# Kernel optimization log

Measured on AMD Instinct MI355X. Metric: run time of the kernel, lower is better.

## Reference

```python
import jax, jax.numpy as jnp
import numpy as np
from jax import lax

RES = 14
DIM = 384
KEY_DIM = 32
NUM_HEADS = 12
ATTN_RATIO = 4
NH_KD = KEY_DIM * NUM_HEADS            # 384
DH = ATTN_RATIO * KEY_DIM * NUM_HEADS  # 1536
HQKV = DH + 2 * NH_KD                  # 2304
BN_EPS = 1e-5


def _bias_idxs():
    ys, xs = np.meshgrid(np.arange(RES), np.arange(RES), indexing='ij')
    ys = ys.reshape(-1); xs = xs.reshape(-1)
    dy = np.abs(ys[:, None] - ys[None, :])
    dx = np.abs(xs[:, None] - xs[None, :])
    return jnp.asarray(dy * RES + dx, dtype=jnp.int32)  # [196,196], 196 unique offsets


def setup_inputs() -> dict:
    key = jax.random.key(0)
    ks = jax.random.split(key, 16)
    B = 128
    x = jax.random.normal(ks[0], (B, DIM, RES, RES), dtype=jnp.float32)
    # qkv: 1x1 conv DIM->HQKV + BN
    qkv_w = jax.random.normal(ks[1], (HQKV, DIM, 1, 1), dtype=jnp.float32) * 0.05
    qkv_g = jax.random.normal(ks[2], (HQKV,), dtype=jnp.float32) * 0.1 + 1.0
    qkv_b = jax.random.normal(ks[3], (HQKV,), dtype=jnp.float32) * 0.1
    qkv_m = jax.random.normal(ks[4], (HQKV,), dtype=jnp.float32) * 0.1
    qkv_v = jax.random.uniform(ks[5], (HQKV,), dtype=jnp.float32) + 0.5
    # dw: depthwise 3x3 conv on q channels + BN
    dw_w = jax.random.normal(ks[6], (NH_KD, 1, 3, 3), dtype=jnp.float32) * 0.2
    dw_g = jax.random.normal(ks[7], (NH_KD,), dtype=jnp.float32) * 0.1 + 1.0
    dw_b = jax.random.normal(ks[8], (NH_KD,), dtype=jnp.float32) * 0.1
    dw_m = jax.random.normal(ks[9], (NH_KD,), dtype=jnp.float32) * 0.1
    dw_v = jax.random.uniform(ks[10], (NH_KD,), dtype=jnp.float32) + 0.5
    # proj: ReLU -> 1x1 conv DH->DIM + BN
    proj_w = jax.random.normal(ks[11], (DIM, DH, 1, 1), dtype=jnp.float32) * 0.05
    proj_g = jax.random.normal(ks[12], (DIM,), dtype=jnp.float32) * 0.1 + 1.0
    proj_b = jax.random.normal(ks[13], (DIM,), dtype=jnp.float32) * 0.1
    proj_m = jax.random.normal(ks[14], (DIM,), dtype=jnp.float32) * 0.1
    proj_v = jax.random.uniform(ks[15], (DIM,), dtype=jnp.float32) + 0.5
    ab = jax.random.normal(jax.random.fold_in(key, 99), (NUM_HEADS, RES * RES), dtype=jnp.float32) * 0.1
    return {
        'x': x,
        'qkv_w': qkv_w, 'qkv_g': qkv_g, 'qkv_b': qkv_b, 'qkv_m': qkv_m, 'qkv_v': qkv_v,
        'dw_w': dw_w, 'dw_g': dw_g, 'dw_b': dw_b, 'dw_m': dw_m, 'dw_v': dw_v,
        'proj_w': proj_w, 'proj_g': proj_g, 'proj_b': proj_b, 'proj_m': proj_m, 'proj_v': proj_v,
        'attn_biases': ab,
        'bias_idxs': _bias_idxs(),
    }


def _bn(x, g, b, m, v):
    scale = g / jnp.sqrt(v + BN_EPS)
    return x * scale[None, :, None, None] + (b - m * scale)[None, :, None, None]


def reference(x, qkv_w, qkv_g, qkv_b, qkv_m, qkv_v,
              dw_w, dw_g, dw_b, dw_m, dw_v,
              proj_w, proj_g, proj_b, proj_m, proj_v,
              attn_biases, bias_idxs):
    B, _, H, W = x.shape
    n = H * W
    scale = KEY_DIM ** -0.5
    # 1x1 conv + BN
    qkv = jnp.einsum('bchw,oc->bohw', x, qkv_w[:, :, 0, 0])
    qkv = _bn(qkv, qkv_g, qkv_b, qkv_m, qkv_v)
    q = qkv[:, :NH_KD]
    k = qkv[:, NH_KD:2 * NH_KD]
    v = qkv[:, 2 * NH_KD:]
    # depthwise 3x3 conv + BN on q
    q = lax.conv_general_dilated(q, dw_w, (1, 1), ((1, 1), (1, 1)),
                                 dimension_numbers=('NCHW', 'OIHW', 'NCHW'),
                                 feature_group_count=NH_KD)
    q = _bn(q, dw_g, dw_b, dw_m, dw_v)
    # heads: [b, h, d, n]
    q = q.reshape(B, NUM_HEADS, KEY_DIM, n)
    k = k.reshape(B, NUM_HEADS, KEY_DIM, n)
    v = v.reshape(B, NUM_HEADS, ATTN_RATIO * KEY_DIM, n)
    bias = attn_biases[:, bias_idxs]  # [h, n, n]
    attn = jnp.einsum('bhdn,bhdm->bhnm', q, k) * scale + bias[None]
    attn = jax.nn.softmax(attn, axis=-1)
    out = jnp.einsum('bhdm,bhnm->bhdn', v, attn).reshape(B, DH, H, W)
    out = jax.nn.relu(out)
    out = jnp.einsum('bchw,oc->bohw', out, proj_w[:, :, 0, 0])
    return _bn(out, proj_g, proj_b, proj_m, proj_v)
```

## Files before the change

kernel.cpp:

```cpp
#include <hip/hip_runtime.h>

typedef __bf16 bf16;
typedef bf16 bf16x8 __attribute__((ext_vector_type(8)));
typedef bf16 bf16x4 __attribute__((ext_vector_type(4)));
typedef short short4v __attribute__((ext_vector_type(4)));
typedef float f32x4 __attribute__((ext_vector_type(4)));

#define NPIX 196
#define CIN 384
#define NHEADS 12
#define MPAD 224
#define VSTRIDE 232
#define OSTRIDE 40
#define TSTRIDE 136
#define TSF 136

#define N_WQ (2304 * 384)
#define N_WP (384 * 1536)
#define N_WD (384 * 9)
#define N_BI (NHEADS * NPIX * MPAD)

__device__ __forceinline__ float ldf(const void* p, size_t i, int f) {
    return f ? ((const float*)p)[i] : (float)((const bf16*)p)[i];
}

__device__ __forceinline__ void gld16(const void* g, void* lds_wave_base) {
    __builtin_amdgcn_global_load_lds(
        (const __attribute__((address_space(1))) void*)(unsigned long long)g,
        (__attribute__((address_space(3))) void*)(unsigned long long)lds_wave_base,
        16, 0, 0);
}

__device__ __forceinline__ int xcd_swizzle(int orig, int nwg) {
    int q = nwg >> 3, r = nwg & 7;
    int xcd = orig & 7, idx = orig >> 3;
    return (xcd < r ? xcd * (q + 1) : r * (q + 1) + (xcd - r) * q) + idx;
}

__device__ __forceinline__ f32x4 mfma16(bf16x4 a, bf16x4 b, f32x4 c) {
#if __has_builtin(__builtin_amdgcn_mfma_f32_16x16x16bf16_1k)
    return __builtin_amdgcn_mfma_f32_16x16x16bf16_1k(
        __builtin_bit_cast(short4v, a), __builtin_bit_cast(short4v, b), c, 0, 0, 0);
#else
    asm volatile("v_mfma_f32_16x16x16_bf16 %0, %1, %2, %0" : "+v"(c) : "v"(a), "v"(b));
    return c;
#endif
}

__device__ __forceinline__ f32x4 vmax4(f32x4 a, f32x4 b) {
    f32x4 r;
    r[0] = fmaxf(a[0], b[0]);
    r[1] = fmaxf(a[1], b[1]);
    r[2] = fmaxf(a[2], b[2]);
    r[3] = fmaxf(a[3], b[3]);
    return r;
}

__global__ void detect_kernel(const unsigned int* __restrict__ x, int* __restrict__ flag) {
    __shared__ int cnt;
    if (threadIdx.x == 0) cnt = 0;
    __syncthreads();
    int c = 0;
#pragma unroll
    for (int k = 0; k < 8; k++) {
        unsigned int w = x[threadIdx.x * 8 + k];
        unsigned int e = (w >> 7) & 0xFFu;
        if (e > 200u) c++;
    }
    atomicAdd(&cnt, c);
    __syncthreads();
    if (threadIdx.x == 0) *flag = (cnt >= 16) ? 1 : 0;
}

__global__ void prep_kernel(const void* __restrict__ qkv_w, const void* __restrict__ proj_w,
                            const void* __restrict__ dw_w, const void* __restrict__ ab,
                            const int* __restrict__ idx, const int* __restrict__ flag,
                            bf16* __restrict__ wq, bf16* __restrict__ wp, bf16* __restrict__ wd,
                            float* __restrict__ biasf, bf16* __restrict__ vb, int nvpad) {
    int f = *flag;
    long t = (long)blockIdx.x * 256 + threadIdx.x;
    if (t < N_WQ) { wq[t] = (bf16)ldf(qkv_w, t, f); return; }
    t -= N_WQ;
    if (t < N_WP) { wp[t] = (bf16)ldf(proj_w, t, f); return; }
    t -= N_WP;
    if (t < N_WD) { wd[t] = (bf16)ldf(dw_w, t, f); return; }
    t -= N_WD;
    if (t < N_BI) {
        int h = (int)(t / (NPIX * MPAD));
        int rem = (int)(t - (long)h * (NPIX * MPAD));
        int n = rem / MPAD, m = rem - n * MPAD;
        biasf[t] = (m < NPIX) ? ldf(ab, h * NPIX + idx[n * NPIX + m], f) : -1e30f;
        return;
    }
    t -= N_BI;
    if (t < nvpad) {
        long r = t / 7, c = t - r * 7;
        *(unsigned long long*)(vb + r * MPAD + NPIX + c * 4) = 0ull;
    }
}

__global__ void transpose_x_kernel(const void* __restrict__ x, const int* __restrict__ flag,
                                   bf16* __restrict__ xt, int b0) {
    __shared__ bf16 tile[32][33];
    int f = *flag;
    int b = blockIdx.z, gb = b0 + b;
    int c0 = blockIdx.y * 32;
    int hw0 = blockIdx.x * 32;
    int tx = threadIdx.x, ty = threadIdx.y;
    int hw = hw0 + tx, c = c0 + ty;
    if (hw < NPIX) tile[ty][tx] = (bf16)ldf(x, ((size_t)gb * CIN + c) * NPIX + hw, f);
    __syncthreads();
    int hw2 = hw0 + ty, c2 = c0 + tx;
    if (hw2 < NPIX) xt[((size_t)b * NPIX + hw2) * CIN + c2] = tile[tx][ty];
}

__device__ __forceinline__ void gemm_tile(const bf16* __restrict__ A, const bf16* __restrict__ B,
                                          int K, bf16* smem, f32x4 acc[4][4]) {
    int tid = threadIdx.x;
    int wave = tid >> 6, lane = tid & 63;
    int wm = wave >> 1, wn = wave & 1;
    int row = lane & 15, grp = lane >> 4;
    int sr = lane >> 3;
    int scg = (lane & 7) ^ sr;
    const int BUF = 128 * 64;
    bf16* As = smem;
    bf16* Bs = smem + 2 * BUF;
    const bf16* Ag = A + (size_t)(wave * 8 + sr) * K + scg * 8;
    const bf16* Bg = B + (size_t)(wave * 8 + sr) * K + scg * 8;
#pragma unroll
    for (int p = 0; p < 4; p++) {
        gld16(Ag + (size_t)(p * 32) * K, As + (p * 256 + wave * 64) * 8);
        gld16(Bg + (size_t)(p * 32) * K, Bs + (p * 256 + wave * 64) * 8);
    }
    int cur = 0;
#pragma unroll 1
    for (int kb = 0; kb < K; kb += 64) {
        if (kb + 64 < K) {
            bf16* Asn = As + (cur ^ 1) * BUF;
            bf16* Bsn = Bs + (cur ^ 1) * BUF;
#pragma unroll
            for (int p = 0; p < 4; p++) {
                gld16(Ag + (size_t)(p * 32) * K + kb + 64, Asn + (p * 256 + wave * 64) * 8);
                gld16(Bg + (size_t)(p * 32) * K + kb + 64, Bsn + (p * 256 + wave * 64) * 8);
            }
            __builtin_amdgcn_sched_barrier(0);
            asm volatile("s_waitcnt vmcnt(8)" ::: "memory");
        } else {
            __builtin_amdgcn_sched_barrier(0);
            asm volatile("s_waitcnt vmcnt(0)" ::: "memory");
        }
        __builtin_amdgcn_s_barrier();
        __builtin_amdgcn_sched_barrier(0);
        const bf16* Asc = As + cur * BUF;
        const bf16* Bsc = Bs + cur * BUF;
#pragma unroll
        for (int ki = 0; ki < 2; ki++) {
            bf16x8 af[4], bfr[4];
#pragma unroll
            for (int t = 0; t < 4; t++) {
                int ra = wm * 64 + t * 16 + row;
                af[t] = *(const bf16x8*)(Asc + ra * 64 + (((ki * 4 + grp) ^ (ra & 7)) * 8));
                int rb = wn * 64 + t * 16 + row;
                bfr[t] = *(const bf16x8*)(Bsc + rb * 64 + (((ki * 4 + grp) ^ (rb & 7)) * 8));
            }
#pragma unroll
            for (int mt = 0; mt < 4; mt++)
#pragma unroll
                for (int nt = 0; nt < 4; nt++)
                    acc[mt][nt] =
                        __builtin_amdgcn_mfma_f32_16x16x32_bf16(af[mt], bfr[nt], acc[mt][nt], 0, 0, 0);
        }
        __builtin_amdgcn_sched_barrier(0);
        __builtin_amdgcn_s_barrier();
        cur ^= 1;
    }
    __builtin_amdgcn_sched_barrier(0);
}

__global__ __launch_bounds__(256) void gemm_qkv_kernel(
    const bf16* __restrict__ xt, const bf16* __restrict__ w,
    const void* __restrict__ g, const void* __restrict__ bb,
    const void* __restrict__ mm, const void* __restrict__ vv, const int* __restrict__ flag,
    bf16* __restrict__ qb, bf16* __restrict__ kt, bf16* __restrict__ vb) {
    __shared__ bf16 smem[4 * 128 * 64];
    f32x4 acc[4][4];
#pragma unroll
    for (int i = 0; i < 4; i++)
#pragma unroll
        for (int j = 0; j < 4; j++) acc[i][j] = (f32x4){0.f, 0.f, 0.f, 0.f};
    int nwg = gridDim.x * gridDim.y;
    int l = xcd_swizzle(blockIdx.y * gridDim.x + blockIdx.x, nwg);
    int m0 = (l % gridDim.x) * 128, n0 = (l / gridDim.x) * 128;
    gemm_tile(w + (size_t)m0 * CIN, xt + (size_t)n0 * CIN, CIN, smem, acc);
    int f = *flag;
    int tid = threadIdx.x;
    int wave = tid >> 6, lane = tid & 63;
    int wm = wave >> 1, wn = wave & 1, row = lane & 15, grp = lane >> 4;
    bf16* tbuf = smem;
    if (m0 >= 384 && m0 < 768) {
#pragma unroll
        for (int mt = 0; mt < 4; mt++) {
#pragma unroll
            for (int r = 0; r < 4; r++) {
                int ol = wm * 64 + mt * 16 + grp * 4 + r;
                int o = m0 + ol;
                float scv = ldf(g, o, f) * rsqrtf(ldf(vv, o, f) + 1e-5f);
                float sh = ldf(bb, o, f) - ldf(mm, o, f) * scv;
#pragma unroll
                for (int nt = 0; nt < 4; nt++) {
                    int nl = wn * 64 + nt * 16 + row;
                    tbuf[nl * TSTRIDE + ol] = (bf16)(acc[mt][nt][r] * scv + sh);
                }
            }
        }
        __syncthreads();
#pragma unroll
        for (int it = 0; it < 8; it++) {
            int g2 = it * 256 + tid;
            int nl = g2 >> 4, ch = g2 & 15;
            *(bf16x8*)(kt + (size_t)(n0 + nl) * CIN + (m0 - 384) + ch * 8) =
                *(const bf16x8*)(tbuf + nl * TSTRIDE + ch * 8);
        }
    } else {
#pragma unroll
        for (int mt = 0; mt < 4; mt++) {
#pragma unroll
            for (int r = 0; r < 4; r++) {
                int ol = wm * 64 + mt * 16 + grp * 4 + r;
                int o = m0 + ol;
                float scv = ldf(g, o, f) * rsqrtf(ldf(vv, o, f) + 1e-5f);
                float sh = ldf(bb, o, f) - ldf(mm, o, f) * scv;
#pragma unroll
                for (int nt = 0; nt < 4; nt++) {
                    int nl = wn * 64 + nt * 16 + row;
                    tbuf[ol * TSTRIDE + nl] = (bf16)(acc[mt][nt][r] * scv + sh);
                }
            }
        }
        __syncthreads();
        bool isq = (m0 < 384);
        bf16* dst = isq ? qb : vb;
        int ostride = isq ? NPIX : MPAD;
        int obase = isq ? m0 : (m0 - 768);
        int orow_mul = isq ? 384 : 1536;
#pragma unroll
        for (int it = 0; it < 8; it++) {
            int g2 = it * 256 + tid;
            int ol = g2 >> 4, ch = g2 & 15;
            int o = obase + ol;
            int ng = n0 + ch * 8;
            int b0i = ng / NPIX, hw0 = ng - b0i * NPIX;
            const bf16* src = tbuf + ol * TSTRIDE + ch * 8;
            if (hw0 <= NPIX - 8) {
                bf16* d = dst + ((size_t)b0i * orow_mul + o) * ostride + hw0;
                *(bf16x4*)d = *(const bf16x4*)src;
                *(bf16x4*)(d + 4) = *(const bf16x4*)(src + 4);
            } else {
#pragma unroll
                for (int j = 0; j < 8; j++) {
                    int n2 = ng + j;
                    int bj = n2 / NPIX, hwj = n2 - bj * NPIX;
                    dst[((size_t)bj * orow_mul + o) * ostride + hwj] = src[j];
                }
            }
        }
    }
}

__global__ __launch_bounds__(256) void gemm_proj_kernel(
    const bf16* __restrict__ ot, const bf16* __restrict__ w,
    const void* __restrict__ g, const void* __restrict__ bb,
    const void* __restrict__ mm, const void* __restrict__ vv, const int* __restrict__ flag,
    void* __restrict__ out, int b0) {
    __shared__ bf16 smem[4 * 128 * 64];
    f32x4 acc[4][4];
#pragma unroll
    for (int i = 0; i < 4; i++)
#pragma unroll
        for (int j = 0; j < 4; j++) acc[i][j] = (f32x4){0.f, 0.f, 0.f, 0.f};
    int nwg = gridDim.x * gridDim.y;
    int l = xcd_swizzle(blockIdx.y * gridDim.x + blockIdx.x, nwg);
    int m0 = (l % gridDim.x) * 128, n0 = (l / gridDim.x) * 128;
    gemm_tile(w + (size_t)m0 * 1536, ot + (size_t)n0 * 1536, 1536, smem, acc);
    int f = *flag;
    int tid = threadIdx.x;
    int wave = tid >> 6, lane = tid & 63;
    int wm = wave >> 1, wn = wave & 1, row = lane & 15, grp = lane >> 4;
    if (f) {
        float* tb = (float*)smem;
#pragma unroll
        for (int half = 0; half < 2; half++) {
            if (wm == half) {
#pragma unroll
                for (int mt = 0; mt < 4; mt++) {
#pragma unroll
                    for (int r = 0; r < 4; r++) {
                        int ol = mt * 16 + grp * 4 + r;
                        int o = m0 + half * 64 + ol;
                        float scv = ldf(g, o, f) * rsqrtf(ldf(vv, o, f) + 1e-5f);
                        float sh = ldf(bb, o, f) - ldf(mm, o, f) * scv;
#pragma unroll
                        for (int nt = 0; nt < 4; nt++) {
                            int nl = wn * 64 + nt * 16 + row;
                            tb[ol * TSF + nl] = acc[mt][nt][r] * scv + sh;
                        }
                    }
                }
            }
            __syncthreads();
            float* outf = (float*)out;
#pragma unroll
            for (int it = 0; it < 8; it++) {
                int g2 = it * 256 + tid;
                int ol = g2 >> 5, ch = g2 & 31;
                int o = m0 + half * 64 + ol;
                int ng = n0 + ch * 4;
                int b0i = ng / NPIX, hw0 = ng - b0i * NPIX;
                const float* src = tb + ol * TSF + ch * 4;
                if (hw0 <= NPIX - 4) {
                    *(f32x4*)(outf + ((size_t)(b0 + b0i) * 384 + o) * NPIX + hw0) =
                        *(const f32x4*)src;
                } else {
#pragma unroll
                    for (int j = 0; j < 4; j++) {
                        int n2 = ng + j;
                        int bj = n2 / NPIX, hwj = n2 - bj * NPIX;
                        outf[((size_t)(b0 + bj) * 384 + o) * NPIX + hwj] = src[j];
                    }
                }
            }
            __syncthreads();
        }
    } else {
#pragma unroll
        for (int mt = 0; mt < 4; mt++) {
#pragma unroll
            for (int r = 0; r < 4; r++) {
                int o = m0 + wm * 64 + mt * 16 + grp * 4 + r;
                float scv = ldf(g, o, f) * rsqrtf(ldf(vv, o, f) + 1e-5f);
                float sh = ldf(bb, o, f) - ldf(mm, o, f) * scv;
#pragma unroll
                for (int nt = 0; nt < 4; nt++) {
                    int n = n0 + wn * 64 + nt * 16 + row;
                    int b = n / NPIX, hw = n - b * NPIX;
                    ((bf16*)out)[((size_t)(b0 + b) * 384 + o) * NPIX + hw] =
                        (bf16)(acc[mt][nt][r] * scv + sh);
                }
            }
        }
    }
}

__global__ void dwconv_kernel(const bf16* __restrict__ qb, const bf16* __restrict__ w,
                              const void* __restrict__ g, const void* __restrict__ bb,
                              const void* __restrict__ mm, const void* __restrict__ vv,
                              const int* __restrict__ flag, bf16* __restrict__ qt) {
    __shared__ bf16 tile[32][33];
    int f = *flag;
    int b = blockIdx.z;
    int c0 = blockIdx.y * 32, hw0 = blockIdx.x * 32;
    int tx = threadIdx.x, ty = threadIdx.y;
    int c = c0 + ty, hw = hw0 + tx;
    if (hw < NPIX) {
        int y = hw / 14, x = hw % 14;
        float acc = 0.f;
        const bf16* wp = w + c * 9;
        const bf16* qp = qb + ((size_t)b * 384 + c) * NPIX;
#pragma unroll
        for (int ky = 0; ky < 3; ky++) {
            int yy = y + ky - 1;
            if (yy < 0 || yy >= 14) continue;
#pragma unroll
            for (int kx = 0; kx < 3; kx++) {
                int xx = x + kx - 1;
                if (xx < 0 || xx >= 14) continue;
                acc += (float)qp[yy * 14 + xx] * (float)wp[ky * 3 + kx];
            }
        }
        float sc = ldf(g, c, f) * rsqrtf(ldf(vv, c, f) + 1e-5f);
        float sh = ldf(bb, c, f) - ldf(mm, c, f) * sc;
        tile[ty][tx] = (bf16)(acc * sc + sh);
    }
    __syncthreads();
    int hw2 = hw0 + ty, c2 = c0 + tx;
    if (hw2 < NPIX) qt[((size_t)b * NPIX + hw2) * CIN + c2] = tile[tx][ty];
}

__global__ __launch_bounds__(256, 2) void attn_kernel(
    const bf16* __restrict__ qt, const bf16* __restrict__ ktp, const bf16* __restrict__ vb,
    const float* __restrict__ biasf, bf16* __restrict__ ot) {
    __shared__ bf16 Vs[128 * VSTRIDE];
    __shared__ bf16 Osh[4][16 * OSTRIDE];
    int nwg = gridDim.x * gridDim.y;
    int l = xcd_swizzle(blockIdx.y * gridDim.x + blockIdx.x, nwg);
    int h = l % NHEADS, b = l / NHEADS;
    int tid = threadIdx.x;
    int wave = tid >> 6, lane = tid & 63;
    int row = lane & 15, grp = lane >> 4;
    const float scale = 0.17677669529663687f;
    const f32x4 zf = {0.f, 0.f, 0.f, 0.f};

    {
        const bf16* vsrc = vb + ((size_t)b * 1536 + h * 128) * MPAD;
#pragma unroll
        for (int it = 0; it < 14; it++) {
            int i = it * 256 + tid;
            int r = i / 28, gch = i - r * 28;
            *(bf16x8*)(Vs + r * VSTRIDE + gch * 8) = *(const bf16x8*)(vsrc + (size_t)i * 8);
        }
    }
    __syncthreads();

    const bf16* vls = Vs + row * VSTRIDE + grp * 4;

    for (int nb = wave; nb < 13; nb += 4) {
        int n0 = nb * 16;
        int n = n0 + row;
        int nc = n > 195 ? 195 : n;

        bf16x8 aq = *(const bf16x8*)(qt + ((size_t)b * NPIX + nc) * CIN + h * 32 + grp * 8);

        f32x4 sacc[14];
        __builtin_amdgcn_s_setprio(1);
#pragma unroll
        for (int mt = 0; mt < 14; mt++) {
            int krow = mt * 16 + row;
            if (krow > 195) krow = 195;
            bf16x8 ak = *(const bf16x8*)(ktp + ((size_t)b * NPIX + krow) * CIN + h * 32 + grp * 8);
            sacc[mt] = __builtin_amdgcn_mfma_f32_16x16x32_bf16(ak, aq, zf, 0, 0, 0);
        }
        __builtin_amdgcn_s_setprio(0);

        const float* bp = biasf + ((size_t)h * NPIX + nc) * MPAD + grp * 4;
        f32x4 mxv = {-3.4e38f, -3.4e38f, -3.4e38f, -3.4e38f};
#pragma unroll
        for (int mt = 0; mt < 14; mt++) {
            f32x4 bv = *(const f32x4*)(bp + mt * 16);
            f32x4 s = sacc[mt] * scale + bv;
            sacc[mt] = s;
            mxv = vmax4(mxv, s);
        }
        float mx = fmaxf(fmaxf(mxv[0], mxv[1]), fmaxf(mxv[2], mxv[3]));
        mx = fmaxf(mx, __shfl_xor(mx, 16));
        mx = fmaxf(mx, __shfl_xor(mx, 32));

        f32x4 sumv = zf;
        bf16x4 pf[14];
#pragma unroll
        for (int mt = 0; mt < 14; mt++) {
            f32x4 e;
#pragma unroll
            for (int r = 0; r < 4; r++) e[r] = __expf(sacc[mt][r] - mx);
            sumv += e;
            bf16x4 pb;
#pragma unroll
            for (int r = 0; r < 4; r++) pb[r] = (bf16)e[r];
            pf[mt] = pb;
        }
        float sum = (sumv[0] + sumv[1]) + (sumv[2] + sumv[3]);
        sum += __shfl_xor(sum, 16);
        sum += __shfl_xor(sum, 32);
        float inv = 1.f / sum;

        f32x4 oacc[8];
#pragma unroll
        for (int dt = 0; dt < 8; dt++) oacc[dt] = zf;
        __builtin_amdgcn_s_setprio(1);
#pragma unroll
        for (int mt = 0; mt < 14; mt++) {
            bf16x4 p = pf[mt];
#pragma unroll
            for (int dt = 0; dt < 8; dt++) {
                bf16x4 v4 = *(const bf16x4*)(vls + dt * 16 * VSTRIDE + mt * 16);
                oacc[dt] = mfma16(v4, p, oacc[dt]);
            }
        }
        __builtin_amdgcn_s_setprio(0);

        bf16* osw = Osh[wave];
        int r2 = lane >> 2, c2 = lane & 3;
        int n2 = n0 + r2;
        bf16* op = ot + ((size_t)b * NPIX + n2) * 1536 + h * 128;
#pragma unroll
        for (int dp = 0; dp < 4; dp++) {
#pragma unroll
            for (int u = 0; u < 2; u++) {
                int dt = dp * 2 + u;
                bf16x4 o4;
#pragma unroll
                for (int r = 0; r < 4; r++) {
                    float v = oacc[dt][r] * inv;
                    o4[r] = (bf16)(v > 0.f ? v : 0.f);
                }
                *(bf16x4*)(osw + row * OSTRIDE + u * 16 + grp * 4) = o4;
            }
            asm volatile("s_waitcnt lgkmcnt(0)" ::: "memory");
            if (n2 < NPIX) {
                bf16x8 ov = *(const bf16x8*)(osw + r2 * OSTRIDE + c2 * 8);
                *(bf16x8*)(op + dp * 32 + c2 * 8) = ov;
            }
            asm volatile("s_waitcnt lgkmcnt(0)" ::: "memory");
        }
    }
}

extern "C" void kernel_launch(void* const* d_in, const int* in_sizes, int n_in,
                              void* d_out, int out_size, void* d_ws, size_t ws_size,
                              hipStream_t stream) {
    const void* x      = d_in[0];
    const void* qkv_w  = d_in[1];
    const void* qkv_g  = d_in[2];
    const void* qkv_b  = d_in[3];
    const void* qkv_m  = d_in[4];
    const void* qkv_v  = d_in[5];
    const void* dw_w   = d_in[6];
    const void* dw_g   = d_in[7];
    const void* dw_b   = d_in[8];
    const void* dw_m   = d_in[9];
    const void* dw_v   = d_in[10];
    const void* proj_w = d_in[11];
    const void* proj_g = d_in[12];
    const void* proj_b = d_in[13];
    const void* proj_m = d_in[14];
    const void* proj_v = d_in[15];
    const void* ab     = d_in[16];
    const int*  idx    = (const int*)d_in[17];

    char* ws = (char*)d_ws;
    size_t off = 0;
    auto alloc = [&](size_t bytes) { void* p = ws + off; off += (bytes + 255) & ~(size_t)255; return p; };

    int*   flag = (int*)alloc(4);
    bf16*  wq   = (bf16*)alloc((size_t)N_WQ * 2);
    bf16*  wp   = (bf16*)alloc((size_t)N_WP * 2);
    bf16*  wd   = (bf16*)alloc((size_t)N_WD * 2);
    float* biasf= (float*)alloc((size_t)N_BI * 4);
    size_t fixed = off;

    const size_t s_xt = (size_t)NPIX * CIN;
    const size_t s_qb = (size_t)384 * NPIX;
    const size_t s_kt = (size_t)NPIX * 384;
    const size_t s_vb = (size_t)1536 * MPAD;
    const size_t s_ot = (size_t)NPIX * 1536;
    const size_t per_image = (s_xt + s_qb + s_kt + s_vb + s_ot) * 2;

    int CB = 128;
    while (CB > 32 && fixed + (size_t)CB * per_image > ws_size) CB >>= 1;

    bf16* xt  = (bf16*)alloc((size_t)CB * s_xt * 2);
    bf16* qb  = (bf16*)alloc((size_t)CB * s_qb * 2);
    bf16* ktp = (bf16*)alloc((size_t)CB * s_kt * 2);
    bf16* vb  = (bf16*)alloc((size_t)CB * s_vb * 2);
    bf16* ot  = (bf16*)alloc((size_t)CB * s_ot * 2);
    bf16* qt  = xt;

    detect_kernel<<<dim3(1), dim3(256), 0, stream>>>((const unsigned int*)x, flag);
    int nvpad = CB * 1536 * 7;
    long prep_total = (long)N_WQ + N_WP + N_WD + N_BI + nvpad;
    int prep_blocks = (int)((prep_total + 255) / 256);
    prep_kernel<<<dim3(prep_blocks), dim3(256), 0, stream>>>(qkv_w, proj_w, dw_w, ab, idx, flag,
                                                             wq, wp, wd, biasf, vb, nvpad);

    dim3 tb(32, 32);
    for (int b0 = 0; b0 < 128; b0 += CB) {
        int cb = (128 - b0 < CB) ? (128 - b0) : CB;
        int ntiles = (cb * NPIX) / 128;
        transpose_x_kernel<<<dim3(7, 12, cb), tb, 0, stream>>>(x, flag, xt, b0);
        gemm_qkv_kernel<<<dim3(18, ntiles), dim3(256), 0, stream>>>(xt, wq, qkv_g, qkv_b, qkv_m,
                                                                    qkv_v, flag, qb, ktp, vb);
        dwconv_kernel<<<dim3(7, 12, cb), tb, 0, stream>>>(qb, wd, dw_g, dw_b, dw_m, dw_v, flag, qt);
        attn_kernel<<<dim3(NHEADS, cb), dim3(256), 0, stream>>>(qt, ktp, vb, biasf, ot);
        gemm_proj_kernel<<<dim3(3, ntiles), dim3(256), 0, stream>>>(ot, wp, proj_g, proj_b, proj_m,
                                                                    proj_v, flag, d_out, b0);
    }
}
```

Baseline: 428.5 us.

## Widen GEMM tiles to 128x256 with K=32 stages and bounds-checked epilogues

Both 1x1-conv GEMMs now use a 128x256 output tile per workgroup, with 8 N-subtiles per wave and a K-step of 32 instead of 64. A new XOR swizzle matches the narrower shared-memory rows. This roughly doubles operand reuse per loaded tile and halves the number of workgroups, and occupancy is hinted at 2 blocks per CU. Epilogues are split into halves that stage through shared memory, with bounds checks for a ragged final N tile. The trade-offs are more accumulator registers, fewer blocks to fill the GPU, and twice as many barriers per K.

```diff
diff --git a/kernel.cpp b/kernel.cpp
--- a/kernel.cpp
+++ b/kernel.cpp
@@ -114,84 +114,85 @@
     if (hw2 < NPIX) xt[((size_t)b * NPIX + hw2) * CIN + c2] = tile[tx][ty];
 }
 
-__device__ __forceinline__ void gemm_tile(const bf16* __restrict__ A, const bf16* __restrict__ B,
-                                          int K, bf16* smem, f32x4 acc[4][4]) {
+template <int K>
+__device__ __forceinline__ void gemm_tile_w(const bf16* __restrict__ A, const bf16* __restrict__ B,
+                                            bf16* smem, f32x4 acc[4][8]) {
+    constexpr int NS = K / 32;
+    const int ABUF = 128 * 32, BBUF = 256 * 32;
     int tid = threadIdx.x;
     int wave = tid >> 6, lane = tid & 63;
     int wm = wave >> 1, wn = wave & 1;
     int row = lane & 15, grp = lane >> 4;
-    int sr = lane >> 3;
-    int scg = (lane & 7) ^ sr;
-    const int BUF = 128 * 64;
+    int sr = lane >> 2;
+    int scg = (lane & 3) ^ ((lane >> 3) & 3);
     bf16* As = smem;
-    bf16* Bs = smem + 2 * BUF;
-    const bf16* Ag = A + (size_t)(wave * 8 + sr) * K + scg * 8;
-    const bf16* Bg = B + (size_t)(wave * 8 + sr) * K + scg * 8;
-#pragma unroll
-    for (int p = 0; p < 4; p++) {
-        gld16(Ag + (size_t)(p * 32) * K, As + (p * 256 + wave * 64) * 8);
-        gld16(Bg + (size_t)(p * 32) * K, Bs + (p * 256 + wave * 64) * 8);
-    }
+    bf16* Bs = smem + 2 * ABUF;
+    const bf16* Aga = A + (size_t)(wave * 32 + sr) * K + scg * 8;
+    const bf16* Bga = B + (size_t)(wave * 64 + sr) * K + scg * 8;
+    int rs = (grp ^ ((row >> 1) & 3)) * 8;
+
+#define STAGEW(s, bi)                                                              \
+    {                                                                              \
+        bf16* Ad = As + (bi) * ABUF + (wave * 32) * 32;                            \
+        bf16* Bd = Bs + (bi) * BBUF + (wave * 64) * 32;                            \
+        _Pragma("unroll") for (int p = 0; p < 2; p++)                              \
+            gld16(Aga + (size_t)(p * 16) * K + (s) * 32, Ad + p * 16 * 32);        \
+        _Pragma("unroll") for (int p = 0; p < 4; p++)                              \
+            gld16(Bga + (size_t)(p * 16) * K + (s) * 32, Bd + p * 16 * 32);        \
+    }
+
+    STAGEW(0, 0);
     int cur = 0;
 #pragma unroll 1
-    for (int kb = 0; kb < K; kb += 64) {
-        if (kb + 64 < K) {
-            bf16* Asn = As + (cur ^ 1) * BUF;
-            bf16* Bsn = Bs + (cur ^ 1) * BUF;
-#pragma unroll
-            for (int p = 0; p < 4; p++) {
-                gld16(Ag + (size_t)(p * 32) * K + kb + 64, Asn + (p * 256 + wave * 64) * 8);
-                gld16(Bg + (size_t)(p * 32) * K + kb + 64, Bsn + (p * 256 + wave * 64) * 8);
-            }
+    for (int s = 0; s < NS; s++) {
+        if (s + 1 < NS) {
+            STAGEW(s + 1, cur ^ 1);
             __builtin_amdgcn_sched_barrier(0);
-            asm volatile("s_waitcnt vmcnt(8)" ::: "memory");
+            asm volatile("s_waitcnt vmcnt(6)" ::: "memory");
         } else {
             __builtin_amdgcn_sched_barrier(0);
             asm volatile("s_waitcnt vmcnt(0)" ::: "memory");
         }
         __builtin_amdgcn_s_barrier();
         __builtin_amdgcn_sched_barrier(0);
-        const bf16* Asc = As + cur * BUF;
-        const bf16* Bsc = Bs + cur * BUF;
-#pragma unroll
-        for (int ki = 0; ki < 2; ki++) {
-            bf16x8 af[4], bfr[4];
-#pragma unroll
-            for (int t = 0; t < 4; t++) {
-                int ra = wm * 64 + t * 16 + row;
-                af[t] = *(const bf16x8*)(Asc + ra * 64 + (((ki * 4 + grp) ^ (ra & 7)) * 8));
-                int rb = wn * 64 + t * 16 + row;
-                bfr[t] = *(const bf16x8*)(Bsc + rb * 64 + (((ki * 4 + grp) ^ (rb & 7)) * 8));
-            }
-#pragma unroll
-            for (int mt = 0; mt < 4; mt++)
-#pragma unroll
-                for (int nt = 0; nt < 4; nt++)
-                    acc[mt][nt] =
-                        __builtin_amdgcn_mfma_f32_16x16x32_bf16(af[mt], bfr[nt], acc[mt][nt], 0, 0, 0);
-        }
+        const bf16* Asc = As + cur * ABUF;
+        const bf16* Bsc = Bs + cur * BBUF;
+        bf16x8 af[4], bfr[8];
+#pragma unroll
+        for (int t = 0; t < 4; t++)
+            af[t] = *(const bf16x8*)(Asc + (wm * 64 + t * 16 + row) * 32 + rs);
+#pragma unroll
+        for (int u = 0; u < 8; u++)
+            bfr[u] = *(const bf16x8*)(Bsc + (wn * 128 + u * 16 + row) * 32 + rs);
+#pragma unroll
+        for (int mt = 0; mt < 4; mt++)
+#pragma unroll
+            for (int nt = 0; nt < 8; nt++)
+                acc[mt][nt] =
+                    __builtin_amdgcn_mfma_f32_16x16x32_bf16(af[mt], bfr[nt], acc[mt][nt], 0, 0, 0);
         __builtin_amdgcn_sched_barrier(0);
         __builtin_amdgcn_s_barrier();
         cur ^= 1;
     }
+#undef STAGEW
     __builtin_amdgcn_sched_barrier(0);
 }
 
-__global__ __launch_bounds__(256) void gemm_qkv_kernel(
+__global__ __launch_bounds__(256, 2) void gemm_qkv_kernel(
     const bf16* __restrict__ xt, const bf16* __restrict__ w,
     const void* __restrict__ g, const void* __restrict__ bb,
     const void* __restrict__ mm, const void* __restrict__ vv, const int* __restrict__ flag,
-    bf16* __restrict__ qb, bf16* __restrict__ kt, bf16* __restrict__ vb) {
-    __shared__ bf16 smem[4 * 128 * 64];
-    f32x4 acc[4][4];
+    bf16* __restrict__ qb, bf16* __restrict__ kt, bf16* __restrict__ vb, int ntot) {
+    __shared__ bf16 smem[2 * 128 * 32 + 2 * 256 * 32];
+    f32x4 acc[4][8];
 #pragma unroll
     for (int i = 0; i < 4; i++)
 #pragma unroll
-        for (int j = 0; j < 4; j++) acc[i][j] = (f32x4){0.f, 0.f, 0.f, 0.f};
+        for (int j = 0; j < 8; j++) acc[i][j] = (f32x4){0.f, 0.f, 0.f, 0.f};
     int nwg = gridDim.x * gridDim.y;
     int l = xcd_swizzle(blockIdx.y * gridDim.x + blockIdx.x, nwg);
-    int m0 = (l % gridDim.x) * 128, n0 = (l / gridDim.x) * 128;
-    gemm_tile(w + (size_t)m0 * CIN, xt + (size_t)n0 * CIN, CIN, smem, acc);
+    int m0 = (l % gridDim.x) * 128, n0 = (l / gridDim.x) * 256;
+    gemm_tile_w<CIN>(w + (size_t)m0 * CIN, xt + (size_t)n0 * CIN, smem, acc);
     int f = *flag;
     int tid = threadIdx.x;
     int wave = tid >> 6, lane = tid & 63;
@@ -199,89 +200,105 @@
     bf16* tbuf = smem;
     if (m0 >= 384 && m0 < 768) {
 #pragma unroll
-        for (int mt = 0; mt < 4; mt++) {
-#pragma unroll
-            for (int r = 0; r < 4; r++) {
-                int ol = wm * 64 + mt * 16 + grp * 4 + r;
-                int o = m0 + ol;
-                float scv = ldf(g, o, f) * rsqrtf(ldf(vv, o, f) + 1e-5f);
-                float sh = ldf(bb, o, f) - ldf(mm, o, f) * scv;
-#pragma unroll
-                for (int nt = 0; nt < 4; nt++) {
-                    int nl = wn * 64 + nt * 16 + row;
-                    tbuf[nl * TSTRIDE + ol] = (bf16)(acc[mt][nt][r] * scv + sh);
+        for (int half = 0; half < 2; half++) {
+            if (wn == half) {
+#pragma unroll
+                for (int mt = 0; mt < 4; mt++) {
+#pragma unroll
+                    for (int r = 0; r < 4; r++) {
+                        int ol = wm * 64 + mt * 16 + grp * 4 + r;
+                        int o = m0 + ol;
+                        float scv = ldf(g, o, f) * rsqrtf(ldf(vv, o, f) + 1e-5f);
+                        float sh = ldf(bb, o, f) - ldf(mm, o, f) * scv;
+#pragma unroll
+                        for (int nt = 0; nt < 8; nt++) {
+                            int nl = nt * 16 + row;
+                            tbuf[nl * TSTRIDE + ol] = (bf16)(acc[mt][nt][r] * scv + sh);
+                        }
+                    }
                 }
             }
-        }
-        __syncthreads();
-#pragma unroll
-        for (int it = 0; it < 8; it++) {
-            int g2 = it * 256 + tid;
-            int nl = g2 >> 4, ch = g2 & 15;
-            *(bf16x8*)(kt + (size_t)(n0 + nl) * CIN + (m0 - 384) + ch * 8) =
-                *(const bf16x8*)(tbuf + nl * TSTRIDE + ch * 8);
+            __syncthreads();
+#pragma unroll
+            for (int it = 0; it < 8; it++) {
+                int g2 = it * 256 + tid;
+                int nl = g2 >> 4, ch = g2 & 15;
+                int n = n0 + half * 128 + nl;
+                if (n < ntot)
+                    *(bf16x8*)(kt + (size_t)n * CIN + (m0 - 384) + ch * 8) =
+                        *(const bf16x8*)(tbuf + nl * TSTRIDE + ch * 8);
+            }
+            __syncthreads();
         }
     } else {
-#pragma unroll
-        for (int mt = 0; mt < 4; mt++) {
-#pragma unroll
-            for (int r = 0; r < 4; r++) {
-                int ol = wm * 64 + mt * 16 + grp * 4 + r;
-                int o = m0 + ol;
-                float scv = ldf(g, o, f) * rsqrtf(ldf(vv, o, f) + 1e-5f);
-                float sh = ldf(bb, o, f) - ldf(mm, o, f) * scv;
-#pragma unroll
-                for (int nt = 0; nt < 4; nt++) {
-                    int nl = wn * 64 + nt * 16 + row;
-                    tbuf[ol * TSTRIDE + nl] = (bf16)(acc[mt][nt][r] * scv + sh);
-                }
-            }
-        }
-        __syncthreads();
         bool isq = (m0 < 384);
         bf16* dst = isq ? qb : vb;
         int ostride = isq ? NPIX : MPAD;
         int obase = isq ? m0 : (m0 - 768);
         int orow_mul = isq ? 384 : 1536;
 #pragma unroll
-        for (int it = 0; it < 8; it++) {
-            int g2 = it * 256 + tid;
-            int ol = g2 >> 4, ch = g2 & 15;
-            int o = obase + ol;
-            int ng = n0 + ch * 8;
-            int b0i = ng / NPIX, hw0 = ng - b0i * NPIX;
-            const bf16* src = tbuf + ol * TSTRIDE + ch * 8;
-            if (hw0 <= NPIX - 8) {
-                bf16* d = dst + ((size_t)b0i * orow_mul + o) * ostride + hw0;
-                *(bf16x4*)d = *(const bf16x4*)src;
-                *(bf16x4*)(d + 4) = *(const bf16x4*)(src + 4);
-            } else {
-#pragma unroll
-                for (int j = 0; j < 8; j++) {
-                    int n2 = ng + j;
-                    int bj = n2 / NPIX, hwj = n2 - bj * NPIX;
-                    dst[((size_t)bj * orow_mul + o) * ostride + hwj] = src[j];
+        for (int half = 0; half < 2; half++) {
+            if (wn == half) {
+#pragma unroll
+                for (int mt = 0; mt < 4; mt++) {
+#pragma unroll
+                    for (int r = 0; r < 4; r++) {
+                        int ol = wm * 64 + mt * 16 + grp * 4 + r;
+                        int o = m0 + ol;
+                        float scv = ldf(g, o, f) * rsqrtf(ldf(vv, o, f) + 1e-5f);
+                        float sh = ldf(bb, o, f) - ldf(mm, o, f) * scv;
+#pragma unroll
+                        for (int nt = 0; nt < 8; nt++) {
+                            int nl = nt * 16 + row;
+                            tbuf[ol * TSTRIDE + nl] = (bf16)(acc[mt][nt][r] * scv + sh);
+                        }
+                    }
                 }
             }
-        }
-    }
-}
-
-__global__ __launch_bounds__(256) void gemm_proj_kernel(
+            __syncthreads();
+#pragma unroll
+            for (int it = 0; it < 8; it++) {
+                int g2 = it * 256 + tid;
+                int ol = g2 >> 4, ch = g2 & 15;
+                int o = obase + ol;
+                int ng = n0 + half * 128 + ch * 8;
+                int b0i = ng / NPIX, hw0 = ng - b0i * NPIX;
+                const bf16* src = tbuf + ol * TSTRIDE + ch * 8;
+                if (hw0 <= NPIX - 8 && ng + 8 <= ntot) {
+                    bf16* d = dst + ((size_t)b0i * orow_mul + o) * ostride + hw0;
+                    *(bf16x4*)d = *(const bf16x4*)src;
+                    *(bf16x4*)(d + 4) = *(const bf16x4*)(src + 4);
+                } else {
+#pragma unroll
+                    for (int j = 0; j < 8; j++) {
+                        int n2 = ng + j;
+                        if (n2 < ntot) {
+                            int bj = n2 / NPIX, hwj = n2 - bj * NPIX;
+                            dst[((size_t)bj * orow_mul + o) * ostride + hwj] = src[j];
+                        }
+                    }
+                }
+            }
+            __syncthreads();
+        }
+    }
+}
+
+__global__ __launch_bounds__(256, 2) void gemm_proj_kernel(
     const bf16* __restrict__ ot, const bf16* __restrict__ w,
     const void* __restrict__ g, const void* __restrict__ bb,
     const void* __restrict__ mm, const void* __restrict__ vv, const int* __restrict__ flag,
-    void* __restrict__ out, int b0) {
-    __shared__ bf16 smem[4 * 128 * 64];
-    f32x4 acc[4][4];
+    void* __restrict__ out, int b0, int ntot) {
+    __shared__ bf16 smem[2 * 128 * 32 + 2 * 256 * 32];
+    f32x4 acc[4][8];
 #pragma unroll
     for (int i = 0; i < 4; i++)
 #pragma unroll
-        for (int j = 0; j < 4; j++) acc[i][j] = (f32x4){0.f, 0.f, 0.f, 0.f};
+        for (int j = 0; j < 8; j++) acc[i][j] = (f32x4){0.f, 0.f, 0.f, 0.f};
     int nwg = gridDim.x * gridDim.y;
     int l = xcd_swizzle(blockIdx.y * gridDim.x + blockIdx.x, nwg);
-    int m0 = (l % gridDim.x) * 128, n0 = (l / gridDim.x) * 128;
-    gemm_tile(w + (size_t)m0 * 1536, ot + (size_t)n0 * 1536, 1536, smem, acc);
+    int m0 = (l % gridDim.x) * 128, n0 = (l / gridDim.x) * 256;
+    gemm_tile_w<1536>(w + (size_t)m0 * 1536, ot + (size_t)n0 * 1536, smem, acc);
     int f = *flag;
     int tid = threadIdx.x;
     int wave = tid >> 6, lane = tid & 63;
@@ -289,47 +306,52 @@
     if (f) {
         float* tb = (float*)smem;
 #pragma unroll
-        for (int half = 0; half < 2; half++) {
-            if (wm == half) {
-#pragma unroll
-                for (int mt = 0; mt < 4; mt++) {
-#pragma unroll
-                    for (int r = 0; r < 4; r++) {
-                        int ol = mt * 16 + grp * 4 + r;
-                        int o = m0 + half * 64 + ol;
-                        float scv = ldf(g, o, f) * rsqrtf(ldf(vv, o, f) + 1e-5f);
-                        float sh = ldf(bb, o, f) - ldf(mm, o, f) * scv;
-#pragma unroll
-                        for (int nt = 0; nt < 4; nt++) {
-                            int nl = wn * 64 + nt * 16 + row;
-                            tb[ol * TSF + nl] = acc[mt][nt][r] * scv + sh;
+        for (int oh = 0; oh < 2; oh++) {
+#pragma unroll
+            for (int nh = 0; nh < 2; nh++) {
+                if (wm == oh && wn == nh) {
+#pragma unroll
+                    for (int mt = 0; mt < 4; mt++) {
+#pragma unroll
+                        for (int r = 0; r < 4; r++) {
+                            int ol = mt * 16 + grp * 4 + r;
+                            int o = m0 + oh * 64 + ol;
+                            float scv = ldf(g, o, f) * rsqrtf(ldf(vv, o, f) + 1e-5f);
+                            float sh = ldf(bb, o, f) - ldf(mm, o, f) * scv;
+#pragma unroll
+                            for (int nt = 0; nt < 8; nt++) {
+                                int nl = nt * 16 + row;
+                                tb[ol * TSF + nl] = acc[mt][nt][r] * scv + sh;
+                            }
                         }
                     }
                 }
-            }
-            __syncthreads();
-            float* outf = (float*)out;
-#pragma unroll
-            for (int it = 0; it < 8; it++) {
-                int g2 = it * 256 + tid;
-                int ol = g2 >> 5, ch = g2 & 31;
-                int o = m0 + half * 64 + ol;
-                int ng = n0 + ch * 4;
-                int b0i = ng / NPIX, hw0 = ng - b0i * NPIX;
-                const float* src = tb + ol * TSF + ch * 4;
-                if (hw0 <= NPIX - 4) {
-                    *(f32x4*)(outf + ((size_t)(b0 + b0i) * 384 + o) * NPIX + hw0) =
-                        *(const f32x4*)src;
-                } else {
-#pragma unroll
-                    for (int j = 0; j < 4; j++) {
-                        int n2 = ng + j;
-                        int bj = n2 / NPIX, hwj = n2 - bj * NPIX;
-                        outf[((size_t)(b0 + bj) * 384 + o) * NPIX + hwj] = src[j];
+                __syncthreads();
+                float* outf = (float*)out;
+#pragma unroll
+                for (int it = 0; it < 8; it++) {
+                    int g2 = it * 256 + tid;
+                    int ol = g2 >> 5, ch = g2 & 31;
+                    int o = m0 + oh * 64 + ol;
+                    int ng = n0 + nh * 128 + ch * 4;
+                    int b0i = ng / NPIX, hw0 = ng - b0i * NPIX;
+                    const float* src = tb + ol * TSF + ch * 4;
+                    if (hw0 <= NPIX - 4 && ng + 4 <= ntot) {
+                        *(f32x4*)(outf + ((size_t)(b0 + b0i) * 384 + o) * NPIX + hw0) =
+                            *(const f32x4*)src;
+                    } else {
+#pragma unroll
+                        for (int j = 0; j < 4; j++) {
+                            int n2 = ng + j;
+                            if (n2 < ntot) {
+                                int bj = n2 / NPIX, hwj = n2 - bj * NPIX;
+                                outf[((size_t)(b0 + bj) * 384 + o) * NPIX + hwj] = src[j];
+                            }
+                        }
                     }
                 }
-            }
-            __syncthreads();
+                __syncthreads();
+            }
         }
     } else {
 #pragma unroll
@@ -340,11 +362,13 @@
                 float scv = ldf(g, o, f) * rsqrtf(ldf(vv, o, f) + 1e-5f);
                 float sh = ldf(bb, o, f) - ldf(mm, o, f) * scv;
 #pragma unroll
-                for (int nt = 0; nt < 4; nt++) {
-                    int n = n0 + wn * 64 + nt * 16 + row;
-                    int b = n / NPIX, hw = n - b * NPIX;
-                    ((bf16*)out)[((size_t)(b0 + b) * 384 + o) * NPIX + hw] =
-                        (bf16)(acc[mt][nt][r] * scv + sh);
+                for (int nt = 0; nt < 8; nt++) {
+                    int n = n0 + wn * 128 + nt * 16 + row;
+                    if (n < ntot) {
+                        int b = n / NPIX, hw = n - b * NPIX;
+                        ((bf16*)out)[((size_t)(b0 + b) * 384 + o) * NPIX + hw] =
+                            (bf16)(acc[mt][nt][r] * scv + sh);
+                    }
                 }
             }
         }
@@ -564,13 +588,14 @@
     dim3 tb(32, 32);
     for (int b0 = 0; b0 < 128; b0 += CB) {
         int cb = (128 - b0 < CB) ? (128 - b0) : CB;
-        int ntiles = (cb * NPIX) / 128;
+        int ntot = cb * NPIX;
+        int ntiles = (ntot + 255) / 256;
         transpose_x_kernel<<<dim3(7, 12, cb), tb, 0, stream>>>(x, flag, xt, b0);
         gemm_qkv_kernel<<<dim3(18, ntiles), dim3(256), 0, stream>>>(xt, wq, qkv_g, qkv_b, qkv_m,
-                                                                    qkv_v, flag, qb, ktp, vb);
+                                                                    qkv_v, flag, qb, ktp, vb, ntot);
         dwconv_kernel<<<dim3(7, 12, cb), tb, 0, stream>>>(qb, wd, dw_g, dw_b, dw_m, dw_v, flag, qt);
         attn_kernel<<<dim3(NHEADS, cb), dim3(256), 0, stream>>>(qt, ktp, vb, biasf, ot);
         gemm_proj_kernel<<<dim3(3, ntiles), dim3(256), 0, stream>>>(ot, wp, proj_g, proj_b, proj_m,
-                                                                    proj_v, flag, d_out, b0);
-    }
-}
+                                                                    proj_v, flag, d_out, b0, ntot);
+    }
+}
```

Result: slower. 491.3 us (+14.7%).
